# Kernel optimization log

Measured on AMD Instinct MI355X. Metric: run time of the kernel, lower is better.

## Reference

```python
import jax, jax.numpy as jnp
import numpy as np


def _lstm_dir(xs, Wih, Whh, bih, bhh, reverse):
    # xs: [T, B, E]; torch LSTM gate order i, f, g, o
    B = xs.shape[1]
    H = Whh.shape[1]
    h0 = jnp.zeros((B, H), xs.dtype)
    c0 = jnp.zeros((B, H), xs.dtype)

    def step(carry, xt):
        h, c = carry
        g = xt @ Wih.T + h @ Whh.T + (bih + bhh)
        i, f, gg, o = jnp.split(g, 4, axis=-1)
        i = jax.nn.sigmoid(i)
        f = jax.nn.sigmoid(f)
        gg = jnp.tanh(gg)
        o = jax.nn.sigmoid(o)
        c_new = f * c + i * gg
        h_new = o * jnp.tanh(c_new)
        return (h_new, c_new), h_new

    _, hs = jax.lax.scan(step, (h0, c0), xs, reverse=reverse)
    return hs  # [T, B, H] time-aligned


def _forward(x, edge_index, emb_table, Wih_f, Whh_f, bih_f, bhh_f,
             Wih_b, Whh_b, bih_b, bhh_b, label_emb, ggc_weight,
             gru_Wih, gru_Whh, gru_bih, gru_bhh, proj_W, proj_b):
    # --- embedding (dropout is identity in eval) ---
    emb = emb_table[x]                       # [B, T, E]
    xs = jnp.transpose(emb, (1, 0, 2))       # [T, B, E]
    hf = _lstm_dir(xs, Wih_f, Whh_f, bih_f, bhh_f, reverse=False)
    hb = _lstm_dir(xs, Wih_b, Whh_b, bih_b, bhh_b, reverse=True)
    c = jnp.concatenate([hf, hb], axis=-1)   # [T, B, 2H]
    c = jnp.transpose(c, (1, 0, 2))          # [B, T, 2H]

    # --- label cosine similarity, summed over tokens ---
    eps = 1e-8
    cn = c / jnp.maximum(jnp.linalg.norm(c, axis=-1, keepdims=True), eps)
    ln = label_emb / jnp.maximum(jnp.linalg.norm(label_emb, axis=-1, keepdims=True), eps)
    ls = jnp.einsum('btd,ld->bl', cn, ln)    # [B, C] (sum over t folded in)

    # --- GatedGraphConv, 2 layers, aggr='add', edge_weight=None ---
    src, dst = edge_index[0], edge_index[1]
    N = ls.shape[0]
    h = ls
    for i in range(ggc_weight.shape[0]):
        m = h @ ggc_weight[i]                            # [N, C]
        m = jax.ops.segment_sum(m[src], dst, num_segments=N)  # gather + scatter-add
        # torch GRUCell: gates r, z, n
        gi = m @ gru_Wih.T + gru_bih
        gh = h @ gru_Whh.T + gru_bhh
        ir, iz, inn = jnp.split(gi, 3, axis=-1)
        hr, hz, hn = jnp.split(gh, 3, axis=-1)
        r = jax.nn.sigmoid(ir + hr)
        z = jax.nn.sigmoid(iz + hz)
        n = jnp.tanh(inn + r * hn)
        h = (1.0 - z) * n + z * h

    return h @ proj_W.T + proj_b             # [B, C]


def setup_inputs() -> dict:
    key = jax.random.key(0)
    ks = jax.random.split(key, 20)
    V, E, B, T, C, NE = 50000, 300, 2048, 64, 1024, 65536
    H = E
    s = 0.05
    inp = {
        'x': jax.random.randint(ks[0], (B, T), 0, V),
        'edge_index': jax.random.randint(ks[1], (2, NE), 0, B),
        'emb_table': jax.random.normal(ks[2], (V, E)) * s,
        'Wih_f': jax.random.normal(ks[3], (4 * H, E)) * s,
        'Whh_f': jax.random.normal(ks[4], (4 * H, H)) * s,
        'bih_f': jnp.zeros((4 * H,)),
        'bhh_f': jnp.zeros((4 * H,)),
        'Wih_b': jax.random.normal(ks[5], (4 * H, E)) * s,
        'Whh_b': jax.random.normal(ks[6], (4 * H, H)) * s,
        'bih_b': jnp.zeros((4 * H,)),
        'bhh_b': jnp.zeros((4 * H,)),
        'label_emb': jax.random.normal(ks[7], (C, 2 * H)) * s,
        'ggc_weight': jax.random.normal(ks[8], (2, C, C)) * (1.0 / np.sqrt(C)),
        'gru_Wih': jax.random.normal(ks[9], (3 * C, C)) * (1.0 / np.sqrt(C)),
        'gru_Whh': jax.random.normal(ks[10], (3 * C, C)) * (1.0 / np.sqrt(C)),
        'gru_bih': jnp.zeros((3 * C,)),
        'gru_bhh': jnp.zeros((3 * C,)),
        'proj_W': jax.random.normal(ks[11], (C, C)) * (1.0 / np.sqrt(C)),
        'proj_b': jnp.zeros((C,)),
    }
    return inp


def reference(x, edge_index, emb_table, Wih_f, Whh_f, bih_f, bhh_f,
              Wih_b, Whh_b, bih_b, bhh_b, label_emb, ggc_weight,
              gru_Wih, gru_Whh, gru_bih, gru_bhh, proj_W, proj_b):
    return _forward(x, edge_index, emb_table, Wih_f, Whh_f, bih_f, bhh_f,
                    Wih_b, Whh_b, bih_b, bhh_b, label_emb, ggc_weight,
                    gru_Wih, gru_Whh, gru_bih, gru_bhh, proj_W, proj_b)
```

## Files before the change

kernel.cpp:

```cpp
#include <hip/hip_runtime.h>
#include <hip/hip_bf16.h>
#include <stdint.h>

typedef __hip_bfloat16 bf16;
typedef __attribute__((ext_vector_type(8))) short frag16;
typedef __attribute__((ext_vector_type(4))) float f32x4;

#define B_ 2048
#define T_ 64
#define E_ 300
#define H_ 300
#define C_ 1024
#define V_ 50000
#define NE_ 65536
#define HP 320
#define KC 640
#define NP 1280

static __device__ __forceinline__ float sigf(float x) {
  x = fminf(fmaxf(x, -30.f), 30.f);
  return 1.f / (1.f + __expf(-x));
}
static __device__ __forceinline__ float tanhfast(float x) {
  x = fminf(fmaxf(x, -15.f), 15.f);
  float e = __expf(2.f * x);
  return (e - 1.f) / (e + 1.f);
}
static __device__ __forceinline__ float ldraw(const void* p, size_t i, int isb) {
  return isb ? __bfloat162float(((const bf16*)p)[i]) : ((const float*)p)[i];
}
static __device__ __forceinline__ short b2s(bf16 b) {
  short s; __builtin_memcpy(&s, &b, 2); return s;
}
static __device__ __forceinline__ short4 f4tob4(float4 v) {
  return make_short4(b2s(__float2bfloat16(v.x)), b2s(__float2bfloat16(v.y)),
                     b2s(__float2bfloat16(v.z)), b2s(__float2bfloat16(v.w)));
}

static __device__ __forceinline__ void g2l16(const void* g, void* l) {
  __builtin_amdgcn_global_load_lds(
      (const __attribute__((address_space(1))) void*)(uintptr_t)g,
      (__attribute__((address_space(3))) void*)(uintptr_t)l, 16, 0, 0);
}

__global__ void detect_dtype(const unsigned short* __restrict__ e2, int* __restrict__ flag) {
  __shared__ int red[4];
  int tid = threadIdx.x;
  int ones = 0;
#pragma unroll
  for (int s = 0; s < 16; ++s) ones += (e2[2 * (tid * 16 + s)] >> 14) & 1;
  for (int off = 32; off > 0; off >>= 1) ones += __shfl_down(ones, off, 64);
  if ((tid & 63) == 0) red[tid >> 6] = ones;
  __syncthreads();
  if (tid == 0) {
    int tot = red[0] + red[1] + red[2] + red[3];
    *flag = (tot < 1024) ? 1 : 0;
  }
}

__global__ __launch_bounds__(256) void gemm_bt(
    const bf16* A, int lda, const bf16* W, int ldw, const float* bias,
    float* Cf, bf16* Cb, int ldc, int K,
    const int* __restrict__ rawp, int outmode,
    const bf16* A2, const bf16* W2, const float* bias2, float* Cf2) {
  if (blockIdx.z) { A = A2; W = W2; bias = bias2; Cf = Cf2; Cb = nullptr; }
  __shared__ __align__(16) short As[2][128 * 32];
  __shared__ __align__(16) short Bs[2][128 * 32];
  const int isb = rawp ? *rawp : 1;
  const int n0 = blockIdx.x * 128, m0 = blockIdx.y * 128;
  const int lane = threadIdx.x & 63, wv = threadIdx.x >> 6;
  const int wm = (wv & 1) * 64, wn = (wv >> 1) * 64;
  const int gr = lane >> 2;
  const int gc = (lane & 3) * 8;
  const short* pA0 = (const short*)A + (size_t)(m0 + wv * 32 + gr) * lda + gc;
  const short* pA1 = pA0 + (size_t)16 * lda;
  const short* pB0 = (const short*)W + (size_t)(n0 + wv * 32 + gr) * ldw + gc;
  const short* pB1 = pB0 + (size_t)16 * ldw;

  auto issueT = [&](int k0, int buf) {
    short* a = &As[buf][wv * 1024];
    short* b = &Bs[buf][wv * 1024];
    g2l16(pA0 + k0, a);
    g2l16(pA1 + k0, a + 512);
    g2l16(pB0 + k0, b);
    g2l16(pB1 + k0, b + 512);
  };

  f32x4 acc[4][4];
#pragma unroll
  for (int i = 0; i < 4; ++i)
#pragma unroll
    for (int j = 0; j < 4; ++j) acc[i][j] = (f32x4){0.f, 0.f, 0.f, 0.f};

  const int nk = K / 32;
  const int krd = (lane >> 4) * 8;
  const int rsel = lane & 15;
  issueT(0, 0);
  if (nk > 1) issueT(32, 1);
  for (int kk = 0; kk < nk; ++kk) {
    const int cur = kk & 1;
    if (kk + 1 < nk) asm volatile("s_waitcnt vmcnt(4)" ::: "memory");
    else asm volatile("s_waitcnt vmcnt(0)" ::: "memory");
    __builtin_amdgcn_s_barrier();
    frag16 af[4], bfg[4];
#pragma unroll
    for (int i = 0; i < 4; ++i) af[i] = *(const frag16*)&As[cur][(wm + i * 16 + rsel) * 32 + krd];
#pragma unroll
    for (int i = 0; i < 4; ++i) bfg[i] = *(const frag16*)&Bs[cur][(wn + i * 16 + rsel) * 32 + krd];
#pragma unroll
    for (int i = 0; i < 4; ++i)
#pragma unroll
      for (int j = 0; j < 4; ++j)
        acc[i][j] = __builtin_amdgcn_mfma_f32_16x16x32_bf16(af[i], bfg[j], acc[i][j], 0, 0, 0);
    asm volatile("" ::: "memory");
    __builtin_amdgcn_s_barrier();
    if (kk + 2 < nk) issueT(32 * (kk + 2), cur);
  }
  const int rq = (lane >> 4) * 4, cq = lane & 15;
#pragma unroll
  for (int j = 0; j < 4; ++j) {
    int cidx = n0 + wn + j * 16 + cq;
    float bv = bias ? bias[cidx] : 0.f;
#pragma unroll
    for (int i = 0; i < 4; ++i) {
      int rbase = m0 + wm + i * 16 + rq;
#pragma unroll
      for (int r = 0; r < 4; ++r) {
        float v = acc[i][j][r] + bv;
        size_t idx = (size_t)(rbase + r) * ldc + cidx;
        if (outmode) {
          if (isb) Cb[idx] = __float2bfloat16(v);
          else Cf[idx] = v;
        } else {
          if (Cf) Cf[idx] = v;
          if (Cb) Cb[idx] = __float2bfloat16(v);
        }
      }
    }
  }
}

static __device__ __forceinline__ void normacc_row2(
    const bf16* hfA, const bf16* hbA, const bf16* hfB, const bf16* hbB,
    float* __restrict__ Spf, int b, int lane) {
  float vA[10], vB[10];
  float sA = 0.f, sB = 0.f;
#pragma unroll
  for (int s = 0; s < 10; ++s) {
    int d = lane + 64 * s;
    float a = 0.f, c = 0.f;
    if (d < 300) {
      a = __bfloat162float(hfA[d]);
      c = __bfloat162float(hfB[d]);
    } else if (d < 600) {
      a = __bfloat162float(hbA[d - 300]);
      c = __bfloat162float(hbB[d - 300]);
    }
    vA[s] = a; vB[s] = c;
    sA += a * a; sB += c * c;
  }
#pragma unroll
  for (int off = 32; off > 0; off >>= 1) {
    sA += __shfl_xor(sA, off, 64);
    sB += __shfl_xor(sB, off, 64);
  }
  float kA = 1.f / fmaxf(sqrtf(sA), 1e-8f);
  float kB = 1.f / fmaxf(sqrtf(sB), 1e-8f);
  float* dst = Spf + (size_t)b * KC;
#pragma unroll
  for (int s = 0; s < 10; ++s) {
    int d = lane + 64 * s;
    if (d < 600) dst[d] += vA[s] * kA + vB[s] * kB;
  }
}

__global__ __launch_bounds__(256) void lstm_step(
    const void* __restrict__ emb, const bf16* __restrict__ embtail,
    const int* __restrict__ x,
    const bf16* __restrict__ Wcat, const float* __restrict__ bcat,
    bf16* __restrict__ hpad, float* __restrict__ cstate,
    bf16* __restrict__ Hfst, bf16* __restrict__ Hbst, float* __restrict__ Spf,
    int s, const int* __restrict__ flagp) {
  const int pb = s & 1;
  const int lane = threadIdx.x & 63, wv = threadIdx.x >> 6;

  if (blockIdx.z == 2) {
    if (s >= 33) {
      int bid = blockIdx.x + gridDim.x * blockIdx.y;
      const bf16* hinf = hpad + (size_t)pb * B_ * HP;
      const bf16* hinb = hpad + (size_t)(2 + pb) * B_ * HP;
      const int t1 = s - 1, t2 = 64 - s;
#pragma unroll
      for (int rep = 0; rep < 2; ++rep) {
        int b = bid * 4 + wv + 1280 * rep;
        if (b < B_)
          normacc_row2(hinf + (size_t)b * HP,
                       Hbst + ((size_t)(t1 - 32) * B_ + b) * H_,
                       Hfst + ((size_t)t2 * B_ + b) * H_,
                       hinb + (size_t)b * HP, Spf, b, lane);
      }
    }
    return;
  }

  __shared__ __align__(16) char smem[24576];
  short* As0 = (short*)smem;
  short* As1 = (short*)(smem + 4096);
  short* Bs0 = (short*)(smem + 8192);
  short* Bs1 = (short*)(smem + 16384);
  float* epi = (float*)smem;

  const int dir = blockIdx.z;
  const int tt = dir ? (T_ - 1 - s) : s;
  const int isb = *flagp;
  const bf16* hin = hpad + (size_t)(dir * 2 + pb) * B_ * HP;
  const bf16* Wd = Wcat + (size_t)dir * NP * KC;
  bf16* hout = hpad + (size_t)(dir * 2 + (1 - pb)) * B_ * HP;
  float* cs = cstate + (size_t)dir * B_ * HP;
  const int n0 = blockIdx.x * 128, m0 = blockIdx.y * 64;
  const int wm = (wv & 1) * 32, wn = (wv >> 1) * 64;
  const int gr = lane >> 2;
  const int gc = (lane & 3) * 8;
  const int arow = m0 + wv * 16 + gr;
  const int tok = x[arow * T_ + tt];
  const short* es = (const short*)emb;
  const float* ef = (const float*)emb;
  const short* px = es + (size_t)tok * E_ + gc;
  const short* ptail = (const short*)embtail + (size_t)tok * 32 + gc;
  const short* ph = (const short*)hin + (size_t)arow * HP + gc;
  const short* pB0 = (const short*)Wd + (size_t)(n0 + wv * 32 + gr) * KC + gc;
  const short* pB1 = pB0 + (size_t)16 * KC;

  auto issueT = [&](int k0, int buf) {
    short* a = (buf ? As1 : As0) + wv * 512;
    short* b = (buf ? Bs1 : Bs0) + wv * 1024;
    if (k0 < HP) {
      g2l16(k0 == 288 ? ptail : (px + k0), a);
    } else {
      g2l16(ph + (k0 - HP), a);
    }
    g2l16(pB0 + k0, b);
    g2l16(pB1 + k0, b + 512);
  };

  f32x4 acc[2][4];
#pragma unroll
  for (int i = 0; i < 2; ++i)
#pragma unroll
    for (int j = 0; j < 4; ++j) acc[i][j] = (f32x4){0.f, 0.f, 0.f, 0.f};

  const int rsel = lane & 15, krd = (lane >> 4) * 8;
  const int NKT = KC / 32;

  auto mfma8 = [&](const short* Ap, const short* Bp) {
    frag16 af[2], bfg[4];
#pragma unroll
    for (int i = 0; i < 2; ++i) af[i] = *(const frag16*)&Ap[(wm + i * 16 + rsel) * 32 + krd];
#pragma unroll
    for (int j = 0; j < 4; ++j) bfg[j] = *(const frag16*)&Bp[(wn + j * 16 + rsel) * 32 + krd];
#pragma unroll
    for (int i = 0; i < 2; ++i)
#pragma unroll
      for (int j = 0; j < 4; ++j)
        acc[i][j] = __builtin_amdgcn_mfma_f32_16x16x32_bf16(af[i], bfg[j], acc[i][j], 0, 0, 0);
  };

  if (isb) {
    issueT(0, 0);
    issueT(32, 1);
    for (int kk = 0; kk < NKT; ++kk) {
      const int cur = kk & 1;
      if (kk + 1 < NKT) asm volatile("s_waitcnt vmcnt(3)" ::: "memory");
      else asm volatile("s_waitcnt vmcnt(0)" ::: "memory");
      __builtin_amdgcn_s_barrier();
      mfma8(cur ? As1 : As0, cur ? Bs1 : Bs0);
      asm volatile("" ::: "memory");
      __builtin_amdgcn_s_barrier();
      if (kk + 2 < NKT) issueT(32 * (kk + 2), cur);
    }
  } else {
    for (int kk = 0; kk < NKT; ++kk) {
      const int k0 = kk * 32;
      if (k0 < HP) {
        int c0 = k0 + gc;
        float4 fa = (c0 < E_) ? *(const float4*)(ef + (size_t)tok * E_ + c0)
                              : make_float4(0.f, 0.f, 0.f, 0.f);
        float4 fb = (c0 + 4 < E_) ? *(const float4*)(ef + (size_t)tok * E_ + c0 + 4)
                                  : make_float4(0.f, 0.f, 0.f, 0.f);
        short* d = As0 + (wv * 16 + gr) * 32 + gc;
        *(short4*)d = f4tob4(fa);
        *(short4*)(d + 4) = f4tob4(fb);
      } else {
        g2l16(ph + (k0 - HP), As0 + wv * 512);
      }
      g2l16(pB0 + k0, Bs0 + wv * 1024);
      g2l16(pB1 + k0, Bs0 + wv * 1024 + 512);
      __syncthreads();
      mfma8(As0, Bs0);
      __syncthreads();
    }
  }

  const int rq = (lane >> 4) * 4, cq = lane & 15;
#pragma unroll
  for (int p = 0; p < 2; ++p) {
    if (wn == p * 64) {
#pragma unroll
      for (int j = 0; j < 4; ++j) {
        int cl = j * 16 + cq;
        float bv = bcat[dir * NP + n0 + p * 64 + cl];
#pragma unroll
        for (int i = 0; i < 2; ++i) {
          int rl = wm + i * 16 + rq;
#pragma unroll
          for (int r = 0; r < 4; ++r) epi[(rl + r) * 64 + cl] = acc[i][j][r] + bv;
        }
      }
    }
    __syncthreads();
    int jbase = (n0 + p * 64) >> 2;
    for (int it = threadIdx.x; it < 64 * 16; it += 256) {
      int rl = it >> 4, jl = it & 15;
      int jg = jbase + jl;
      if (jg < H_) {
        const float* row = epi + rl * 64 + jl * 4;
        float iv = sigf(row[0]);
        float fv = sigf(row[1]);
        float gv = tanhfast(row[2]);
        float ov = sigf(row[3]);
        int b = m0 + rl;
        float c = fv * cs[(size_t)b * HP + jg] + iv * gv;
        float h = ov * tanhfast(c);
        cs[(size_t)b * HP + jg] = c;
        bf16 hb = __float2bfloat16(h);
        hout[(size_t)b * HP + jg] = hb;
        if (dir) {
          if (tt >= 32) Hbst[((size_t)(tt - 32) * B_ + b) * H_ + jg] = hb;
        } else if (tt < 32) {
          Hfst[((size_t)tt * B_ + b) * H_ + jg] = hb;
        }
      }
    }
    __syncthreads();
  }
}

__global__ __launch_bounds__(256) void normacc_fin(const bf16* __restrict__ hpad,
                                                   const bf16* __restrict__ Hfst,
                                                   const bf16* __restrict__ Hbst,
                                                   float* __restrict__ Spf) {
  int b = blockIdx.x * 4 + (threadIdx.x >> 6);
  int lane = threadIdx.x & 63;
  normacc_row2(hpad + (size_t)b * HP,
               Hbst + ((size_t)31 * B_ + b) * H_,
               Hfst + (size_t)b * H_,
               hpad + (size_t)2 * B_ * HP + (size_t)b * HP, Spf, b, lane);
}

__global__ void prep_all(const void* __restrict__ Wih_f, const void* __restrict__ Whh_f,
                         const void* __restrict__ bih_f, const void* __restrict__ bhh_f,
                         const void* __restrict__ Wih_b, const void* __restrict__ Whh_b,
                         const void* __restrict__ bih_b, const void* __restrict__ bhh_b,
                         const void* __restrict__ label, const void* __restrict__ ggcw,
                         const void* __restrict__ emb,
                         bf16* __restrict__ Wcat, float* __restrict__ bcat,
                         bf16* __restrict__ lnp, bf16* __restrict__ ggct,
                         bf16* __restrict__ embtail,
                         const int* __restrict__ flagp) {
  const int isb = *flagp;
  if (blockIdx.x < 1024) {
    int l = blockIdx.x, tid = threadIdx.x;
    __shared__ float red[4];
    float v[3];
    float ss = 0.f;
#pragma unroll
    for (int s = 0; s < 3; ++s) {
      int d = tid + 256 * s;
      v[s] = (d < 600) ? ldraw(label, (size_t)l * 600 + d, isb) : 0.f;
      ss += v[s] * v[s];
    }
    for (int off = 32; off > 0; off >>= 1) ss += __shfl_down(ss, off, 64);
    if ((tid & 63) == 0) red[tid >> 6] = ss;
    __syncthreads();
    float scale = 1.f / fmaxf(sqrtf(red[0] + red[1] + red[2] + red[3]), 1e-8f);
#pragma unroll
    for (int s = 0; s < 3; ++s) {
      int d = tid + 256 * s;
      if (d < KC) lnp[(size_t)l * KC + d] = __float2bfloat16(v[s] * scale);
    }
    return;
  }
  int i = (blockIdx.x - 1024) * 256 + threadIdx.x;
  if (i < 2 * NP * KC) {
    int k = i % KC;
    int n = (i / KC) % NP;
    int dir = i / (KC * NP);
    int j = n >> 2, q = n & 3;
    const void* Wih = dir ? Wih_b : Wih_f;
    const void* Whh = dir ? Whh_b : Whh_f;
    float v = 0.f;
    if (j < H_) {
      int row = q * H_ + j;
      if (k < E_) v = ldraw(Wih, (size_t)row * E_ + k, isb);
      else if (k >= HP && k < HP + H_) v = ldraw(Whh, (size_t)row * H_ + (k - HP), isb);
    }
    Wcat[i] = __float2bfloat16(v);
    if (k == 0) {
      const void* bih = dir ? bih_b : bih_f;
      const void* bhh = dir ? bhh_b : bhh_f;
      bcat[dir * NP + n] =
          (j < H_) ? (ldraw(bih, q * H_ + j, isb) + ldraw(bhh, q * H_ + j, isb)) : 0.f;
    }
    return;
  }
  i -= 2 * NP * KC;
  if (i < 2 * C_ * C_) {
    int k = i & 1023, n = (i >> 10) & 1023, l = i >> 20;
    size_t src = ((size_t)l << 20) | ((size_t)k << 10) | (size_t)n;
    ggct[i] = __float2bfloat16(ldraw(ggcw, src, isb));
    return;
  }
  i -= 2 * C_ * C_;
  if (i < V_ * 32) {
    int v = i >> 5, c = i & 31;
    float val = (c < E_ - 288) ? ldraw(emb, (size_t)v * E_ + 288 + c, isb) : 0.f;
    embtail[i] = __float2bfloat16(val);
  }
}

__global__ void prep2(const void* __restrict__ gWih, const void* __restrict__ gWhh,
                      const void* __restrict__ projW, const void* __restrict__ gbih,
                      const void* __restrict__ gbhh, const void* __restrict__ projb,
                      bf16* __restrict__ gWihb, bf16* __restrict__ gWhhb,
                      bf16* __restrict__ projWb, float* __restrict__ gbihf,
                      float* __restrict__ gbhhf, float* __restrict__ projbf,
                      const int* __restrict__ flagp) {
  const int isb = *flagp;
  int i = blockIdx.x * 256 + threadIdx.x;
  if (i < 3072 * C_) { gWihb[i] = __float2bfloat16(ldraw(gWih, i, isb)); return; }
  i -= 3072 * C_;
  if (i < 3072 * C_) { gWhhb[i] = __float2bfloat16(ldraw(gWhh, i, isb)); return; }
  i -= 3072 * C_;
  if (i < C_ * C_) { projWb[i] = __float2bfloat16(ldraw(projW, i, isb)); return; }
  i -= C_ * C_;
  if (i < 3072) { gbihf[i] = ldraw(gbih, i, isb); return; }
  i -= 3072;
  if (i < 3072) { gbhhf[i] = ldraw(gbhh, i, isb); return; }
  i -= 3072;
  if (i < C_) { projbf[i] = ldraw(projb, i, isb); }
}

__global__ void zero_u4(uint4* __restrict__ p, int n16) {
  int i = blockIdx.x * 256 + threadIdx.x;
  if (i < n16) p[i] = make_uint4(0u, 0u, 0u, 0u);
}

__global__ void edge_cnt(const int* __restrict__ ei, int* __restrict__ cnt) {
  int e = blockIdx.x * 256 + threadIdx.x;
  if (e < NE_) {
    int s = ei[e], d = ei[NE_ + e];
    atomicAdd(&cnt[(size_t)d * B_ + s], 1);
  }
}
__global__ void cnt2bf(const int* __restrict__ cnt, bf16* __restrict__ A) {
  int i = blockIdx.x * 256 + threadIdx.x;
  A[i] = __float2bfloat16((float)cnt[i]);
}

__global__ void gru_ew(const float* __restrict__ gi, const float* __restrict__ gh,
                       float* __restrict__ h, bf16* __restrict__ hb16) {
  int i = blockIdx.x * 256 + threadIdx.x;
  int b = i >> 10, j = i & 1023;
  const float* gib = gi + (size_t)b * 3072;
  const float* ghb = gh + (size_t)b * 3072;
  float r = sigf(gib[j] + ghb[j]);
  float z = sigf(gib[1024 + j] + ghb[1024 + j]);
  float n = tanhfast(gib[2048 + j] + r * ghb[2048 + j]);
  float hv = (1.f - z) * n + z * h[i];
  h[i] = hv;
  hb16[i] = __float2bfloat16(hv);
}

__global__ void spcvt(const float* __restrict__ Spf, bf16* __restrict__ Sp) {
  int i = blockIdx.x * 256 + threadIdx.x;
  Sp[i] = __float2bfloat16(Spf[i]);
}

__global__ void sentinel(bf16* __restrict__ o, int n, float v) {
  int i = blockIdx.x * 256 + threadIdx.x;
  if (i < n) o[i] = __float2bfloat16(v);
}

extern "C" void kernel_launch(void* const* d_in, const int* in_sizes, int n_in,
                              void* d_out, int out_size, void* d_ws, size_t ws_size,
                              hipStream_t stream) {
  const int* x = (const int*)d_in[0];
  const int* ei = (const int*)d_in[1];
  const void* emb = d_in[2];
  const void* Wih_f = d_in[3];
  const void* Whh_f = d_in[4];
  const void* bih_f = d_in[5];
  const void* bhh_f = d_in[6];
  const void* Wih_b = d_in[7];
  const void* Whh_b = d_in[8];
  const void* bih_b = d_in[9];
  const void* bhh_b = d_in[10];
  const void* label = d_in[11];
  const void* ggcw = d_in[12];
  const void* gWih = d_in[13];
  const void* gWhh = d_in[14];
  const void* gbih = d_in[15];
  const void* gbhh = d_in[16];
  const void* projW = d_in[17];
  const void* projb = d_in[18];
  (void)in_sizes; (void)n_in;

  const size_t NEED = (size_t)112 * 1024 * 1024;
  if (ws_size < NEED) {
    float v = 100.f + (float)(ws_size >> 24);
    sentinel<<<(out_size + 255) / 256, 256, 0, stream>>>((bf16*)d_out, out_size, v);
    return;
  }

  char* w = (char*)d_ws;
  size_t off = 0;
  auto alloc = [&](size_t bytes) {
    char* p = w + off;
    off += (bytes + 255) & ~(size_t)255;
    return p;
  };
  int* dflag = (int*)alloc(256);
  bf16* Wcat = (bf16*)alloc((size_t)2 * NP * KC * 2);
  float* bcat = (float*)alloc((size_t)2 * NP * 4);
  bf16* lnp = (bf16*)alloc((size_t)C_ * KC * 2);
  bf16* ggct = (bf16*)alloc((size_t)2 * C_ * C_ * 2);
  bf16* Sp = (bf16*)alloc((size_t)B_ * KC * 2);
  bf16* embtail = (bf16*)alloc((size_t)V_ * 32 * 2);
  const size_t phase_base = off;
  float* Spf = (float*)alloc((size_t)B_ * KC * 4);
  bf16* hpad = (bf16*)alloc((size_t)4 * B_ * HP * 2);
  float* cst = (float*)alloc((size_t)2 * B_ * HP * 4);
  bf16* Hfst = (bf16*)alloc((size_t)32 * B_ * H_ * 2);
  bf16* Hbst = (bf16*)alloc((size_t)32 * B_ * H_ * 2);
  off = phase_base;
  float* hbuf = (float*)alloc((size_t)B_ * C_ * 4);
  bf16* hb16 = (bf16*)alloc((size_t)B_ * C_ * 2);
  bf16* m1t = (bf16*)alloc((size_t)C_ * B_ * 2);
  bf16* aggb = (bf16*)alloc((size_t)B_ * C_ * 2);
  bf16* Acnt = (bf16*)alloc((size_t)B_ * B_ * 2);
  float* gi = (float*)alloc((size_t)B_ * 3072 * 4);
  float* gh = (float*)alloc((size_t)B_ * 3072 * 4);
  bf16* gWihb = (bf16*)alloc((size_t)3072 * C_ * 2);
  bf16* gWhhb = (bf16*)alloc((size_t)3072 * C_ * 2);
  bf16* projWb = (bf16*)alloc((size_t)C_ * C_ * 2);
  float* gbihf = (float*)alloc(3072 * 4);
  float* gbhhf = (float*)alloc(3072 * 4);
  float* projbf = (float*)alloc(C_ * 4);
  int* cnt = (int*)gi;

  detect_dtype<<<1, 256, 0, stream>>>((const unsigned short*)emb, dflag);
  prep_all<<<1024 + (2 * NP * KC + 2 * C_ * C_ + V_ * 32) / 256, 256, 0, stream>>>(
      Wih_f, Whh_f, bih_f, bhh_f, Wih_b, Whh_b, bih_b, bhh_b, label, ggcw, emb,
      Wcat, bcat, lnp, ggct, embtail, dflag);
  zero_u4<<<(3 * 327680) / 256, 256, 0, stream>>>((uint4*)Spf, 3 * 327680);

  for (int s = 0; s < T_; ++s)
    lstm_step<<<dim3(NP / 128, B_ / 64, 3), 256, 0, stream>>>(emb, embtail, x, Wcat, bcat,
                                                              hpad, cst, Hfst, Hbst, Spf,
                                                              s, dflag);
  normacc_fin<<<B_ / 4, 256, 0, stream>>>(hpad, Hfst, Hbst, Spf);
  spcvt<<<(B_ * KC) / 256, 256, 0, stream>>>(Spf, Sp);

  prep2<<<(2 * 3072 * C_ + C_ * C_ + 2 * 3072 + C_) / 256, 256, 0, stream>>>(
      gWih, gWhh, projW, gbih, gbhh, projb, gWihb, gWhhb, projWb, gbihf, gbhhf, projbf, dflag);

  gemm_bt<<<dim3(C_ / 128, B_ / 128), 256, 0, stream>>>(Sp, KC, lnp, KC, nullptr,
                                                        hbuf, hb16, C_, KC, nullptr, 0,
                                                        nullptr, nullptr, nullptr, nullptr);
  zero_u4<<<(B_ * B_ * 4 / 16) / 256, 256, 0, stream>>>((uint4*)cnt, B_ * B_ * 4 / 16);
  edge_cnt<<<NE_ / 256, 256, 0, stream>>>(ei, cnt);
  cnt2bf<<<(B_ * B_) / 256, 256, 0, stream>>>(cnt, Acnt);
  for (int l = 0; l < 2; ++l) {
    gemm_bt<<<dim3(B_ / 128, C_ / 128), 256, 0, stream>>>(ggct + (size_t)l * C_ * C_, C_,
                                                          hb16, C_, nullptr,
                                                          nullptr, m1t, B_, C_, nullptr, 0,
                                                          nullptr, nullptr, nullptr, nullptr);
    gemm_bt<<<dim3(C_ / 128, B_ / 128), 256, 0, stream>>>(Acnt, B_, m1t, B_, nullptr,
                                                          nullptr, aggb, C_, B_, nullptr, 0,
                                                          nullptr, nullptr, nullptr, nullptr);
    gemm_bt<<<dim3(3072 / 128, B_ / 128, 2), 256, 0, stream>>>(aggb, C_, gWihb, C_, gbihf,
                                                               gi, nullptr, 3072, C_, nullptr, 0,
                                                               hb16, gWhhb, gbhhf, gh);
    gru_ew<<<(B_ * C_) / 256, 256, 0, stream>>>(gi, gh, hbuf, hb16);
  }
  gemm_bt<<<dim3(C_ / 128, B_ / 128), 256, 0, stream>>>(hb16, C_, projWb, C_, projbf,
                                                        (float*)d_out, (bf16*)d_out, C_, C_,
                                                        dflag, 1,
                                                        nullptr, nullptr, nullptr, nullptr);
}
```

Baseline: 2.226 ms.

## Triple-buffer LDS tiles and swizzle block order in GEMM and LSTM step kernels

Both the generic bf16 GEMM and the fused LSTM step kernel move from double to triple buffering of LDS tiles. This keeps two K-tiles of global loads in flight, and the vmcnt waits are adjusted to match. Block indices are also remapped so that groups of 8 consecutive blocks share weight or activation tiles, aiming for better L2 reuse. The cost is more shared memory per block, which may lower occupancy, and the remap assumes the grid dimensions divide evenly by 8.

```diff
diff --git a/kernel.cpp b/kernel.cpp
--- a/kernel.cpp
+++ b/kernel.cpp
@@ -64,10 +64,16 @@
     const int* __restrict__ rawp, int outmode,
     const bf16* A2, const bf16* W2, const float* bias2, float* Cf2) {
   if (blockIdx.z) { A = A2; W = W2; bias = bias2; Cf = Cf2; Cb = nullptr; }
-  __shared__ __align__(16) short As[2][128 * 32];
-  __shared__ __align__(16) short Bs[2][128 * 32];
+  __shared__ __align__(16) short As[3][128 * 32];
+  __shared__ __align__(16) short Bs[3][128 * 32];
   const int isb = rawp ? *rawp : 1;
-  const int n0 = blockIdx.x * 128, m0 = blockIdx.y * 128;
+  const int nxb = gridDim.x;
+  const int id = blockIdx.x + nxb * blockIdx.y;
+  const int npx = nxb >> 3;
+  const int jj = id >> 3;
+  const int bx = (id & 7) * npx + (npx > 1 ? jj % npx : 0);
+  const int by = npx > 1 ? jj / npx : jj;
+  const int n0 = bx * 128, m0 = by * 128;
   const int lane = threadIdx.x & 63, wv = threadIdx.x >> 6;
   const int wm = (wv & 1) * 64, wn = (wv >> 1) * 64;
   const int gr = lane >> 2;
@@ -97,10 +103,12 @@
   const int rsel = lane & 15;
   issueT(0, 0);
   if (nk > 1) issueT(32, 1);
+  if (nk > 2) issueT(64, 2);
   for (int kk = 0; kk < nk; ++kk) {
-    const int cur = kk & 1;
-    if (kk + 1 < nk) asm volatile("s_waitcnt vmcnt(4)" ::: "memory");
-    else asm volatile("s_waitcnt vmcnt(0)" ::: "memory");
+    const int cur = kk % 3;
+    if (kk + 2 < nk)      asm volatile("s_waitcnt vmcnt(8)" ::: "memory");
+    else if (kk + 1 < nk) asm volatile("s_waitcnt vmcnt(4)" ::: "memory");
+    else                  asm volatile("s_waitcnt vmcnt(0)" ::: "memory");
     __builtin_amdgcn_s_barrier();
     frag16 af[4], bfg[4];
 #pragma unroll
@@ -114,7 +122,7 @@
         acc[i][j] = __builtin_amdgcn_mfma_f32_16x16x32_bf16(af[i], bfg[j], acc[i][j], 0, 0, 0);
     asm volatile("" ::: "memory");
     __builtin_amdgcn_s_barrier();
-    if (kk + 2 < nk) issueT(32 * (kk + 2), cur);
+    if (kk + 3 < nk) issueT(32 * (kk + 3), cur);
   }
   const int rq = (lane >> 4) * 4, cq = lane & 15;
 #pragma unroll
@@ -203,11 +211,7 @@
     return;
   }
 
-  __shared__ __align__(16) char smem[24576];
-  short* As0 = (short*)smem;
-  short* As1 = (short*)(smem + 4096);
-  short* Bs0 = (short*)(smem + 8192);
-  short* Bs1 = (short*)(smem + 16384);
+  __shared__ __align__(16) char smem[36864];
   float* epi = (float*)smem;
 
   const int dir = blockIdx.z;
@@ -217,7 +221,11 @@
   const bf16* Wd = Wcat + (size_t)dir * NP * KC;
   bf16* hout = hpad + (size_t)(dir * 2 + (1 - pb)) * B_ * HP;
   float* cs = cstate + (size_t)dir * B_ * HP;
-  const int n0 = blockIdx.x * 128, m0 = blockIdx.y * 64;
+  const int id = blockIdx.x + gridDim.x * blockIdx.y;
+  const int jj = id >> 3;
+  const int mt = (id & 7) * 4 + (jj & 3);
+  const int nt = jj >> 2;
+  const int n0 = nt * 128, m0 = mt * 64;
   const int wm = (wv & 1) * 32, wn = (wv >> 1) * 64;
   const int gr = lane >> 2;
   const int gc = (lane & 3) * 8;
@@ -232,8 +240,8 @@
   const short* pB1 = pB0 + (size_t)16 * KC;
 
   auto issueT = [&](int k0, int buf) {
-    short* a = (buf ? As1 : As0) + wv * 512;
-    short* b = (buf ? Bs1 : Bs0) + wv * 1024;
+    short* a = (short*)(smem + buf * 4096) + wv * 512;
+    short* b = (short*)(smem + 12288 + buf * 8192) + wv * 1024;
     if (k0 < HP) {
       g2l16(k0 == 288 ? ptail : (px + k0), a);
     } else {
@@ -268,17 +276,21 @@
   if (isb) {
     issueT(0, 0);
     issueT(32, 1);
+    issueT(64, 2);
     for (int kk = 0; kk < NKT; ++kk) {
-      const int cur = kk & 1;
-      if (kk + 1 < NKT) asm volatile("s_waitcnt vmcnt(3)" ::: "memory");
-      else asm volatile("s_waitcnt vmcnt(0)" ::: "memory");
+      const int cur = kk % 3;
+      if (kk + 2 < NKT)      asm volatile("s_waitcnt vmcnt(6)" ::: "memory");
+      else if (kk + 1 < NKT) asm volatile("s_waitcnt vmcnt(3)" ::: "memory");
+      else                   asm volatile("s_waitcnt vmcnt(0)" ::: "memory");
       __builtin_amdgcn_s_barrier();
-      mfma8(cur ? As1 : As0, cur ? Bs1 : Bs0);
+      mfma8((const short*)(smem + cur * 4096), (const short*)(smem + 12288 + cur * 8192));
       asm volatile("" ::: "memory");
       __builtin_amdgcn_s_barrier();
-      if (kk + 2 < NKT) issueT(32 * (kk + 2), cur);
+      if (kk + 3 < NKT) issueT(32 * (kk + 3), cur);
     }
   } else {
+    short* As0 = (short*)smem;
+    short* Bs0 = (short*)(smem + 12288);
     for (int kk = 0; kk < NKT; ++kk) {
       const int k0 = kk * 32;
       if (k0 < HP) {
```

After: 1.967 ms. -11.6%, faster.
